# Optimization experiments

Measured on AMD Instinct MI355X. Metric: run time of the kernel, lower is better.

Reference implementation:

```python
import jax, jax.numpy as jnp
import numpy as np

TOP_N = 16

def pairwise_l2(q, c):
    # Euclidean distance via ||q||^2 + ||c||^2 - 2 q.c, matching torch.cdist(p=2)
    qn = jnp.sum(q * q, axis=-1, keepdims=True)        # [B,S,1]
    cn = jnp.sum(c * c, axis=-1)[:, None, :]           # [B,1,C]
    d2 = qn + cn - 2.0 * jnp.einsum('bsd,bcd->bsc', q, c)
    return jnp.sqrt(jnp.maximum(d2, 0.0))

def setup_inputs() -> dict:
    key = jax.random.key(0)
    k1, k2, k3, k4, k5 = jax.random.split(key, 5)
    B, S, C, K, D = 4, 1024, 4096, 64, 256
    return {
        'query_embeddings': jax.random.normal(k1, (B, S, D), jnp.float32),
        'context_embeddings': jax.random.normal(k2, (B, C, D), jnp.float32),
        'memory_embeddings': jax.random.normal(k3, (B, K, D), jnp.float32),
        'W': jax.random.normal(k4, (D, D), jnp.float32) / jnp.sqrt(jnp.float32(D)),
        'b': jax.random.normal(k5, (D,), jnp.float32) * 0.01,
    }

def reference(query_embeddings, context_embeddings, memory_embeddings, W, b):
    # latent_query_projection (nn.Linear): x @ W^T + b
    qp = jnp.einsum('bsd,ed->bse', query_embeddings, W) + b
    d_ctx = pairwise_l2(qp, context_embeddings)                       # [B,S,C]
    mem = memory_embeddings.reshape(memory_embeddings.shape[0], -1,
                                    memory_embeddings.shape[-1])
    d_mem = pairwise_l2(qp, mem)                                      # [B,S,K]
    distances = jnp.concatenate([d_ctx, d_mem], axis=-1)              # [B,S,C+K]
    neg_top, idx = jax.lax.top_k(-distances, TOP_N)                   # smallest distances
    return -neg_top, idx
```

## Files before the change

### kernel.cpp

```cpp
#include <hip/hip_runtime.h>
#include <hip/hip_bf16.h>
#include <cfloat>
#include <cmath>

#define B_ 4
#define S_ 1024
#define C_ 4096
#define K_ 64
#define D_ 256
#define NC 4160
#define TOPN 16
#define NSPLIT 8
#define CANDK 128

typedef __attribute__((ext_vector_type(8))) short short8;
typedef __attribute__((ext_vector_type(4))) float f32x4;

#define UMIN(a, b) ((a) < (b) ? (a) : (b))
#define UMAX(a, b) ((a) < (b) ? (b) : (a))

__global__ __launch_bounds__(256) void prep_kernel(
    const float* __restrict__ q, const float* __restrict__ W,
    const float* __restrict__ bias, double* __restrict__ qp64,
    __hip_bfloat16* __restrict__ qpb,
    const float* __restrict__ ctx, const float* __restrict__ mem,
    unsigned short* __restrict__ candb, float* __restrict__ cn)
{
  __shared__ alignas(16) float As[32][36];
  __shared__ alignas(16) float Ws[64][36];
  const int blk = blockIdx.x;
  const int tid = threadIdx.x;

  if (blk < 512) {
    const int m0 = (blk >> 2) * 32;
    const int n0 = (blk & 3) * 64;
    const int tx = tid & 15;
    const int ty = tid >> 4;
    const int lr = tid >> 3;
    const int lk = (tid & 7) * 4;
    double acc[2][4] = {};
    for (int k0 = 0; k0 < D_; k0 += 32) {
      __syncthreads();
      {
        float4 a0 = *(const float4*)&q[(size_t)(m0 + lr) * D_ + k0 + lk];
        *(float4*)&As[lr][lk] = a0;
        float4 w0 = *(const float4*)&W[(size_t)(n0 + lr) * D_ + k0 + lk];
        float4 w1 = *(const float4*)&W[(size_t)(n0 + lr + 32) * D_ + k0 + lk];
        *(float4*)&Ws[lr][lk] = w0;
        *(float4*)&Ws[lr + 32][lk] = w1;
      }
      __syncthreads();
      #pragma unroll
      for (int kk = 0; kk < 32; kk += 4) {
        float4 av[2], wv[4];
        #pragma unroll
        for (int i = 0; i < 2; ++i) av[i] = *(const float4*)&As[ty * 2 + i][kk];
        #pragma unroll
        for (int j = 0; j < 4; ++j) wv[j] = *(const float4*)&Ws[tx + 16 * j][kk];
        #pragma unroll
        for (int i = 0; i < 2; ++i)
          #pragma unroll
          for (int j = 0; j < 4; ++j) {
            acc[i][j] = fma((double)av[i].x, (double)wv[j].x, acc[i][j]);
            acc[i][j] = fma((double)av[i].y, (double)wv[j].y, acc[i][j]);
            acc[i][j] = fma((double)av[i].z, (double)wv[j].z, acc[i][j]);
            acc[i][j] = fma((double)av[i].w, (double)wv[j].w, acc[i][j]);
          }
      }
    }
    #pragma unroll
    for (int i = 0; i < 2; ++i) {
      const int m = m0 + ty * 2 + i;
      #pragma unroll
      for (int j = 0; j < 4; ++j) {
        const int n = n0 + tx + 16 * j;
        const double v = acc[i][j] + (double)bias[n];
        qp64[(size_t)m * D_ + n] = v;
        qpb[(size_t)m * D_ + n] = __float2bfloat16((float)v);
      }
    }
    return;
  }

  const float* src;
  int e4, log2rpb, row_base;
  if (blk < 512 + 4096) { src = ctx; e4 = (blk - 512) * 256 + tid; log2rpb = 12; row_base = 0; }
  else                  { src = mem; e4 = (blk - 4608) * 256 + tid; log2rpb = 6; row_base = C_; }
  const int row = e4 >> 6;
  const int b = row >> log2rpb;
  const int r = row & ((1 << log2rpb) - 1);
  const int k4 = e4 & 63;
  const float4 v = ((const float4*)src)[e4];
  const int R = row_base + r;
  const int g = R >> 4, l15 = R & 15;
  const int k = k4 * 4;
  const int s = k >> 5, lg = (k & 31) >> 3, ii = k & 7;
  unsigned short* d = candb + (size_t)b * (NC * D_) +
                      (size_t)g * 4096 + s * 512 + lg * 128 + l15 * 8 + ii;
  ushort4 o;
  __hip_bfloat16 h0 = __float2bfloat16(v.x); o.x = *(unsigned short*)&h0;
  __hip_bfloat16 h1 = __float2bfloat16(v.y); o.y = *(unsigned short*)&h1;
  __hip_bfloat16 h2 = __float2bfloat16(v.z); o.z = *(unsigned short*)&h2;
  __hip_bfloat16 h3 = __float2bfloat16(v.w); o.w = *(unsigned short*)&h3;
  *(ushort4*)d = o;
  float sacc = v.x * v.x + v.y * v.y + v.z * v.z + v.w * v.w;
  #pragma unroll
  for (int off = 32; off > 0; off >>= 1) sacc += __shfl_down(sacc, off);
  if ((tid & 63) == 0) cn[b * NC + row_base + r] = sacc;
}

#define INSERT_CANDS(ACC, CBASE)                                              \
  {                                                                           \
    const float4 cn4 = *(const float4*)&cnb[(CBASE) + lg * 4];                \
    unsigned k0, k1, k2, k3;                                                  \
    {                                                                         \
      unsigned kk[4];                                                         \
      _Pragma("unroll")                                                       \
      for (int r = 0; r < 4; ++r) {                                           \
        const float d2v = fmaf(-2.0f, (ACC)[r], ((const float*)&cn4)[r]);     \
        kk[r] = (__float_as_uint(d2v) & 0xFFFFE000u)                          \
                | (unsigned)((CBASE) + lg * 4 + r);                           \
      }                                                                       \
      unsigned t;                                                             \
      t = UMIN(kk[0], kk[1]); kk[1] = UMAX(kk[0], kk[1]); kk[0] = t;          \
      t = UMIN(kk[2], kk[3]); kk[3] = UMAX(kk[2], kk[3]); kk[2] = t;          \
      t = UMIN(kk[0], kk[2]); kk[2] = UMAX(kk[0], kk[2]); kk[0] = t;          \
      t = UMIN(kk[1], kk[3]); kk[3] = UMAX(kk[1], kk[3]); kk[1] = t;          \
      t = UMIN(kk[1], kk[2]); kk[2] = UMAX(kk[1], kk[2]); kk[1] = t;          \
      k0 = kk[0]; k1 = kk[1]; k2 = kk[2]; k3 = kk[3];                         \
    }                                                                         \
    unsigned nl[16];                                                          \
    nl[0] = UMIN(ld[0], k0);                                                  \
    nl[1] = UMIN(UMIN(ld[1], UMAX(ld[0], k0)), k1);                           \
    nl[2] = UMIN(UMIN(ld[2], UMAX(ld[1], k0)),                                \
                 UMIN(UMAX(ld[0], k1), k2));                                  \
    nl[3] = UMIN(UMIN(UMIN(ld[3], UMAX(ld[2], k0)),                           \
                      UMIN(UMAX(ld[1], k1), UMAX(ld[0], k2))), k3);           \
    _Pragma("unroll")                                                         \
    for (int i = 4; i < 16; ++i) {                                            \
      nl[i] = UMIN(UMIN(UMIN(ld[i], UMAX(ld[i - 1], k0)),                     \
                        UMIN(UMAX(ld[i - 2], k1), UMAX(ld[i - 3], k2))),      \
                   UMAX(ld[i - 4], k3));                                      \
    }                                                                         \
    _Pragma("unroll")                                                         \
    for (int i = 0; i < 16; ++i) ld[i] = nl[i];                               \
  }

#define MFMA_CHAIN(ACC, FRAGS)                                                \
  f32x4 ACC;                                                                  \
  {                                                                           \
    f32x4 c0_ = {0.f,0.f,0.f,0.f}, c1_ = {0.f,0.f,0.f,0.f};                   \
    f32x4 c2_ = {0.f,0.f,0.f,0.f}, c3_ = {0.f,0.f,0.f,0.f};                   \
    c0_ = __builtin_amdgcn_mfma_f32_16x16x32_bf16((FRAGS)[0], bfr[0], c0_, 0, 0, 0); \
    c1_ = __builtin_amdgcn_mfma_f32_16x16x32_bf16((FRAGS)[1], bfr[1], c1_, 0, 0, 0); \
    c2_ = __builtin_amdgcn_mfma_f32_16x16x32_bf16((FRAGS)[2], bfr[2], c2_, 0, 0, 0); \
    c3_ = __builtin_amdgcn_mfma_f32_16x16x32_bf16((FRAGS)[3], bfr[3], c3_, 0, 0, 0); \
    c0_ = __builtin_amdgcn_mfma_f32_16x16x32_bf16((FRAGS)[4], bfr[4], c0_, 0, 0, 0); \
    c1_ = __builtin_amdgcn_mfma_f32_16x16x32_bf16((FRAGS)[5], bfr[5], c1_, 0, 0, 0); \
    c2_ = __builtin_amdgcn_mfma_f32_16x16x32_bf16((FRAGS)[6], bfr[6], c2_, 0, 0, 0); \
    c3_ = __builtin_amdgcn_mfma_f32_16x16x32_bf16((FRAGS)[7], bfr[7], c3_, 0, 0, 0); \
    ACC = (c0_ + c1_) + (c2_ + c3_);                                          \
  }

__global__ __launch_bounds__(256) void dist_topk_kernel(
    const __hip_bfloat16* __restrict__ qpb, const unsigned short* __restrict__ candb,
    const float* __restrict__ cn, unsigned* __restrict__ topidx)
{
  const int b = blockIdx.x & 3;
  const int split = (blockIdx.x >> 2) & 7;
  const int rt = blockIdx.x >> 5;
  const int row0 = rt * 16;
  const int tid = threadIdx.x;
  const int w = tid >> 6;
  const int lane = tid & 63;
  const int l15 = lane & 15;
  const int lg = lane >> 4;

  __shared__ unsigned md[16][16][17];

  short8 bfr[8];
  {
    const short* qrow = (const short*)qpb + ((size_t)(b * S_ + row0 + l15)) * D_ + lg * 8;
    #pragma unroll
    for (int s = 0; s < 8; ++s) bfr[s] = *(const short8*)(qrow + s * 32);
  }

  const float* cnb = cn + b * NC;
  const short* cbp = (const short*)candb + (size_t)b * NC * D_ + lg * 128 + l15 * 8;

  unsigned ld[16];
  #pragma unroll
  for (int i = 0; i < TOPN; ++i) ld[i] = 0xFFFFFFFFu;

  const bool has_tail = (w == 3 && split < 4);
  const int gtail = 256 + split;

  short8 aA[8], aB[8];
  #pragma unroll
  for (int s = 0; s < 8; ++s)
    aA[s] = *(const short8*)(cbp + (size_t)(split + 8 * w) * 4096 + s * 512);

  for (int j = 0; j < 4; ++j) {
    const int gA = split + 8 * (w + 8 * j);
    const int gB = gA + 32;
    #pragma unroll
    for (int s = 0; s < 8; ++s)
      aB[s] = *(const short8*)(cbp + (size_t)gB * 4096 + s * 512);

    MFMA_CHAIN(acc, aA);

    if (j < 3) {
      #pragma unroll
      for (int s = 0; s < 8; ++s)
        aA[s] = *(const short8*)(cbp + (size_t)(gA + 64) * 4096 + s * 512);
    } else if (has_tail) {
      #pragma unroll
      for (int s = 0; s < 8; ++s)
        aA[s] = *(const short8*)(cbp + (size_t)gtail * 4096 + s * 512);
    }

    MFMA_CHAIN(acc2, aB);

    INSERT_CANDS(acc, gA * 16);
    INSERT_CANDS(acc2, gB * 16);
  }
  if (has_tail) {
    MFMA_CHAIN(acc, aA);
    INSERT_CANDS(acc, gtail * 16);
  }

  const int lid = w * 4 + lg;
  #pragma unroll
  for (int i = 0; i < TOPN; ++i) md[l15][lid][i] = ld[i];
  __syncthreads();

  {
    const int g = lane >> 4;
    const int h = l15;
    const int row = w * 4 + g;
    int ptr = 0;
    unsigned cur = md[row][h][0];
    unsigned mykey = 0xFFFFFFFFu;
    #pragma unroll
    for (int it = 0; it < TOPN; ++it) {
      unsigned m = cur;
      #pragma unroll
      for (int off = 8; off > 0; off >>= 1) {
        const unsigned o = __shfl_xor(m, off, 16);
        m = (o < m) ? o : m;
      }
      if (h == it) mykey = m;
      if (cur == m) {
        ++ptr;
        cur = (ptr < TOPN) ? md[row][h][ptr] : 0xFFFFFFFFu;
      }
    }
    unsigned* dst = topidx + ((size_t)(b * S_ + row0 + row)) * CANDK + split * TOPN;
    dst[h] = mykey;
  }
}

__global__ __launch_bounds__(256) void refine_kernel(
    const double* __restrict__ qp64, const float* __restrict__ ctx,
    const float* __restrict__ mem, const unsigned* __restrict__ topidx,
    float* __restrict__ out)
{
  const int row_global = blockIdx.x;
  const int tid = threadIdx.x;
  const int w = tid >> 6;
  const int lane = tid & 63;
  const int c2 = lane >> 5;
  const int ll = lane & 31;
  const int b = row_global >> 10;

  __shared__ unsigned sA[64], sB[64];
  __shared__ double d2s[64];
  __shared__ int    ids_s[64];

  if (w < 2) {
    unsigned key = topidx[(size_t)row_global * CANDK + w * 64 + lane];
    #pragma unroll
    for (int k = 2; k <= 64; k <<= 1) {
      #pragma unroll
      for (int j2 = k >> 1; j2 > 0; j2 >>= 1) {
        const unsigned o = __shfl_xor(key, j2);
        const bool up = ((lane & k) == 0);
        const bool keep_min = (((lane & j2) == 0) == up);
        const bool less = key < o;
        if (keep_min ? !less : less) key = o;
      }
    }
    if (w == 0) sA[lane] = key; else sB[lane] = key;
  }
  if (w == 2 && lane < 32) { d2s[32 + lane] = DBL_MAX; ids_s[32 + lane] = 0x7fffffff; }
  __syncthreads();

  const double* qrow = qp64 + (size_t)row_global * D_;
  double qd[8];
  #pragma unroll
  for (int t = 0; t < 8; t += 2) {
    double2 v = *(const double2*)&qrow[ll * 8 + t];
    qd[t] = v.x; qd[t + 1] = v.y;
  }

  int cis[4]; float4 cva[4], cvb[4];
  #pragma unroll
  for (int j = 0; j < 4; ++j) {
    const int p = w * 8 + 2 * j + c2;
    const unsigned kk = UMIN(sA[p], sB[31 - p]);
    cis[j] = (int)(kk & 0x1FFFu);
  }
  #pragma unroll
  for (int j = 0; j < 4; ++j) {
    const int ci = cis[j];
    const float* cp = (ci < C_) ? ctx + ((size_t)b * C_ + ci) * D_
                                : mem + ((size_t)b * K_ + (ci - C_)) * D_;
    cva[j] = *(const float4*)&cp[ll * 8];
    cvb[j] = *(const float4*)&cp[ll * 8 + 4];
  }

  #pragma unroll
  for (int j = 0; j < 4; ++j) {
    double a0 = 0.0, a1 = 0.0, df;
    df = qd[0] - (double)cva[j].x; a0 = fma(df, df, a0);
    df = qd[1] - (double)cva[j].y; a1 = fma(df, df, a1);
    df = qd[2] - (double)cva[j].z; a0 = fma(df, df, a0);
    df = qd[3] - (double)cva[j].w; a1 = fma(df, df, a1);
    df = qd[4] - (double)cvb[j].x; a0 = fma(df, df, a0);
    df = qd[5] - (double)cvb[j].y; a1 = fma(df, df, a1);
    df = qd[6] - (double)cvb[j].z; a0 = fma(df, df, a0);
    df = qd[7] - (double)cvb[j].w; a1 = fma(df, df, a1);
    double acc = a0 + a1;
    #pragma unroll
    for (int off = 16; off > 0; off >>= 1) acc += __shfl_down(acc, off, 32);
    if (ll == 0) { d2s[w * 8 + 2 * j + c2] = acc; ids_s[w * 8 + 2 * j + c2] = cis[j]; }
  }
  __syncthreads();

  if (w == 0) {
    double d2 = d2s[lane];
    int    ci = ids_s[lane];
    #pragma unroll
    for (int k = 2; k <= 64; k <<= 1) {
      #pragma unroll
      for (int j2 = k >> 1; j2 > 0; j2 >>= 1) {
        const double od2 = __shfl_xor(d2, j2);
        const int    oci = __shfl_xor(ci, j2);
        const bool up = ((lane & k) == 0);
        const bool less = (d2 < od2) || (d2 == od2 && ci < oci);
        const bool keep_min = (((lane & j2) == 0) == up);
        const bool take = keep_min ? !less : less;
        if (take) { d2 = od2; ci = oci; }
      }
    }
    if (lane < TOPN) {
      const size_t obase = (size_t)row_global * TOPN;
      out[obase + lane] = (float)sqrt(d2 < 0.0 ? 0.0 : d2);
      out[(size_t)B_ * S_ * TOPN + obase + lane] = (float)ci;
    }
  }
}

extern "C" void kernel_launch(void* const* d_in, const int* in_sizes, int n_in,
                              void* d_out, int out_size, void* d_ws, size_t ws_size,
                              hipStream_t stream) {
  const float* q    = (const float*)d_in[0];
  const float* ctx  = (const float*)d_in[1];
  const float* mem  = (const float*)d_in[2];
  const float* W    = (const float*)d_in[3];
  const float* bias = (const float*)d_in[4];
  float* out = (float*)d_out;

  double* qp64 = (double*)d_ws;
  __hip_bfloat16* qpb = (__hip_bfloat16*)(qp64 + (size_t)B_ * S_ * D_);
  unsigned short* candb = (unsigned short*)(qpb + (size_t)B_ * S_ * D_);
  float* cn    = (float*)(candb + (size_t)B_ * NC * D_);
  unsigned* topidx = (unsigned*)(cn + (size_t)B_ * NC);

  prep_kernel<<<4672, 256, 0, stream>>>(q, W, bias, qp64, qpb, ctx, mem, candb, cn);
  dist_topk_kernel<<<2048, 256, 0, stream>>>(qpb, candb, cn, topidx);
  refine_kernel<<<B_ * S_, 256, 0, stream>>>(qp64, ctx, mem, topidx, out);
}
```

Before: 86.72 us.

## Share candidate tiles across four row-tile waves via double-buffered LDS

The distance/top-k kernel now gives each wave its own 16-row query tile, four per block, so a block covers 64 rows instead of 16. Candidate bf16 tiles are staged cooperatively into double-buffered shared memory and reused by all four waves. This cuts global or L2 reads of candidates by four and the grid from 2048 to 512 blocks. It adds LDS traffic, a barrier per step and a smaller grid, which may leave compute units underused and reduce latency hiding.

Measured after the change: 78.55 us. 9.4% less time.

```diff
diff --git a/kernel.cpp b/kernel.cpp
--- a/kernel.cpp
+++ b/kernel.cpp
@@ -168,15 +168,16 @@
 {
   const int b = blockIdx.x & 3;
   const int split = (blockIdx.x >> 2) & 7;
-  const int rt = blockIdx.x >> 5;
-  const int row0 = rt * 16;
+  const int rq = blockIdx.x >> 5;
   const int tid = threadIdx.x;
   const int w = tid >> 6;
   const int lane = tid & 63;
   const int l15 = lane & 15;
   const int lg = lane >> 4;
-
-  __shared__ unsigned md[16][16][17];
+  const int row0 = rq * 64 + w * 16;
+
+  __shared__ short sbuf[2][2][4096];
+  __shared__ unsigned md[4][16][4][17];
 
   short8 bfr[8];
   {
@@ -186,77 +187,88 @@
   }
 
   const float* cnb = cn + b * NC;
-  const short* cbp = (const short*)candb + (size_t)b * NC * D_ + lg * 128 + l15 * 8;
+  const short* cbase = (const short*)candb + (size_t)b * NC * D_;
 
   unsigned ld[16];
   #pragma unroll
   for (int i = 0; i < TOPN; ++i) ld[i] = 0xFFFFFFFFu;
 
-  const bool has_tail = (w == 3 && split < 4);
-  const int gtail = 256 + split;
-
-  short8 aA[8], aB[8];
-  #pragma unroll
-  for (int s = 0; s < 8; ++s)
-    aA[s] = *(const short8*)(cbp + (size_t)(split + 8 * w) * 4096 + s * 512);
-
-  for (int j = 0; j < 4; ++j) {
-    const int gA = split + 8 * (w + 8 * j);
-    const int gB = gA + 32;
-    #pragma unroll
-    for (int s = 0; s < 8; ++s)
-      aB[s] = *(const short8*)(cbp + (size_t)gB * 4096 + s * 512);
-
-    MFMA_CHAIN(acc, aA);
-
-    if (j < 3) {
+  short8 vS[2][2];
+  #pragma unroll
+  for (int i = 0; i < 2; ++i)
+    #pragma unroll
+    for (int h = 0; h < 2; ++h)
+      vS[i][h] = *(const short8*)(cbase + (size_t)(split + 8 * i) * 4096 +
+                                  h * 2048 + tid * 8);
+  #pragma unroll
+  for (int i = 0; i < 2; ++i)
+    #pragma unroll
+    for (int h = 0; h < 2; ++h)
+      *(short8*)&sbuf[0][i][h * 2048 + tid * 8] = vS[i][h];
+
+  #pragma unroll 1
+  for (int c = 0; c < 16; ++c) {
+    if (c < 15) {
+      #pragma unroll
+      for (int i = 0; i < 2; ++i)
+        #pragma unroll
+        for (int h = 0; h < 2; ++h)
+          vS[i][h] = *(const short8*)(cbase +
+                       (size_t)(split + 8 * (2 * (c + 1) + i)) * 4096 +
+                       h * 2048 + tid * 8);
+    }
+    __syncthreads();
+    #pragma unroll
+    for (int i = 0; i < 2; ++i) {
+      short8 fr[8];
       #pragma unroll
       for (int s = 0; s < 8; ++s)
-        aA[s] = *(const short8*)(cbp + (size_t)(gA + 64) * 4096 + s * 512);
-    } else if (has_tail) {
-      #pragma unroll
-      for (int s = 0; s < 8; ++s)
-        aA[s] = *(const short8*)(cbp + (size_t)gtail * 4096 + s * 512);
-    }
-
-    MFMA_CHAIN(acc2, aB);
-
-    INSERT_CANDS(acc, gA * 16);
-    INSERT_CANDS(acc2, gB * 16);
-  }
-  if (has_tail) {
-    MFMA_CHAIN(acc, aA);
-    INSERT_CANDS(acc, gtail * 16);
-  }
-
-  const int lid = w * 4 + lg;
-  #pragma unroll
-  for (int i = 0; i < TOPN; ++i) md[l15][lid][i] = ld[i];
+        fr[s] = *(const short8*)&sbuf[c & 1][i][s * 512 + lane * 8];
+      MFMA_CHAIN(acc, fr);
+      INSERT_CANDS(acc, (split + 8 * (2 * c + i)) * 16);
+    }
+    if (c < 15) {
+      #pragma unroll
+      for (int i = 0; i < 2; ++i)
+        #pragma unroll
+        for (int h = 0; h < 2; ++h)
+          *(short8*)&sbuf[(c + 1) & 1][i][h * 2048 + tid * 8] = vS[i][h];
+    }
+  }
+
+  if (split < 4) {
+    const short* p = cbase + (size_t)(256 + split) * 4096 + lane * 8;
+    short8 fr[8];
+    #pragma unroll
+    for (int s = 0; s < 8; ++s) fr[s] = *(const short8*)(p + s * 512);
+    MFMA_CHAIN(acc, fr);
+    INSERT_CANDS(acc, (256 + split) * 16);
+  }
+
+  #pragma unroll
+  for (int i = 0; i < TOPN; ++i) md[w][l15][lg][i] = ld[i];
   __syncthreads();
 
   {
-    const int g = lane >> 4;
-    const int h = l15;
-    const int row = w * 4 + g;
+    const int r = lane >> 2;
+    const int h = lane & 3;
     int ptr = 0;
-    unsigned cur = md[row][h][0];
-    unsigned mykey = 0xFFFFFFFFu;
+    unsigned cur = md[w][r][h][0];
+    unsigned mk[4];
     #pragma unroll
     for (int it = 0; it < TOPN; ++it) {
-      unsigned m = cur;
-      #pragma unroll
-      for (int off = 8; off > 0; off >>= 1) {
-        const unsigned o = __shfl_xor(m, off, 16);
-        m = (o < m) ? o : m;
-      }
-      if (h == it) mykey = m;
+      unsigned m = cur, o;
+      o = __shfl_xor(m, 1, 4); m = o < m ? o : m;
+      o = __shfl_xor(m, 2, 4); m = o < m ? o : m;
+      if ((it & 3) == h) mk[it >> 2] = m;
       if (cur == m) {
         ++ptr;
-        cur = (ptr < TOPN) ? md[row][h][ptr] : 0xFFFFFFFFu;
-      }
-    }
-    unsigned* dst = topidx + ((size_t)(b * S_ + row0 + row)) * CANDK + split * TOPN;
-    dst[h] = mykey;
+        cur = (ptr < TOPN) ? md[w][r][h][ptr] : 0xFFFFFFFFu;
+      }
+    }
+    unsigned* dst = topidx + ((size_t)(b * S_ + row0 + r)) * CANDK + split * TOPN;
+    #pragma unroll
+    for (int k2 = 0; k2 < 4; ++k2) dst[4 * k2 + h] = mk[k2];
   }
 }
 
@@ -378,6 +390,6 @@
   unsigned* topidx = (unsigned*)(cn + (size_t)B_ * NC);
 
   prep_kernel<<<4672, 256, 0, stream>>>(q, W, bias, qp64, qpb, ctx, mem, candb, cn);
-  dist_topk_kernel<<<2048, 256, 0, stream>>>(qpb, candb, cn, topidx);
+  dist_topk_kernel<<<512, 256, 0, stream>>>(qpb, candb, cn, topidx);
   refine_kernel<<<B_ * S_, 256, 0, stream>>>(qp64, ctx, mem, topidx, out);
 }
```
